# Optimization experiments

Measured on AMD Instinct MI355X. Metric: run time of the kernel, lower is better.

## Reference

```python
import jax, jax.numpy as jnp
import numpy as np

B, L, D_IN, D_MODEL, H = 8, 1024, 256, 512, 8
D_HEAD = D_MODEL // H


def setup_inputs() -> dict:
    key = jax.random.key(0)
    ks = jax.random.split(key, 12)
    queries = jax.random.normal(ks[0], (B, L, D_IN), dtype=jnp.float32)
    keys_ = jax.random.normal(ks[1], (B, L, D_IN), dtype=jnp.float32)
    values = jax.random.normal(ks[2], (B, L, D_IN), dtype=jnp.float32)
    attention_mask = jnp.ones((B, L), dtype=jnp.int32)
    # binary symmetric-ish adjacency (sparse molecular graph style)
    adjacency_matrix = (jax.random.uniform(ks[3], (B, L, L)) < 0.05).astype(jnp.float32)
    distance_matrix = jax.random.uniform(ks[4], (B, L, L), dtype=jnp.float32) * 10.0
    s = 1.0 / np.sqrt(D_IN)
    W_q = jax.random.normal(ks[5], (D_MODEL, D_IN), dtype=jnp.float32) * s
    W_k = jax.random.normal(ks[6], (D_MODEL, D_IN), dtype=jnp.float32) * s
    W_v = jax.random.normal(ks[7], (D_MODEL, D_IN), dtype=jnp.float32) * s
    W_o = jax.random.normal(ks[8], (D_MODEL, D_MODEL), dtype=jnp.float32) / np.sqrt(D_MODEL)
    lambda_a = jax.random.normal(ks[9], (H,), dtype=jnp.float32) * 0.1
    lambda_d = jax.random.normal(ks[10], (H,), dtype=jnp.float32) * 0.1
    return {"queries": queries, "keys": keys_, "values": values,
            "attention_mask": attention_mask, "adjacency_matrix": adjacency_matrix,
            "distance_matrix": distance_matrix, "W_q": W_q, "W_k": W_k,
            "W_v": W_v, "W_o": W_o, "lambda_a": lambda_a, "lambda_d": lambda_d}


def _split_heads(x):
    # (b, l, d_model) -> (b, h, l, d_head)
    b, l, _ = x.shape
    return x.reshape(b, l, H, D_HEAD).transpose(0, 2, 1, 3)


def reference(queries, keys, values, attention_mask, adjacency_matrix,
              distance_matrix, W_q, W_k, W_v, W_o, lambda_a, lambda_d):
    Q = _split_heads(queries @ W_q.T)   # (b,h,l,d)
    K = _split_heads(keys @ W_k.T)
    V = _split_heads(values @ W_v.T)
    scores = jnp.einsum("bhqd,bhkd->bhqk", Q, K) / jnp.sqrt(jnp.asarray(D_HEAD, Q.dtype))
    # MSRSA: per-head learned scalars inject graph structure into the scores
    scores = (scores
              + lambda_a[None, :, None, None] * adjacency_matrix[:, None, :, :]
              + lambda_d[None, :, None, None] * distance_matrix[:, None, :, :])
    mask = attention_mask[:, None, None, :] > 0  # (b,1,1,l) key mask
    scores = jnp.where(mask, scores, jnp.asarray(-1e9, scores.dtype))
    attn_weight = jax.nn.softmax(scores, axis=-1)  # (b,h,l,l)
    out = jnp.einsum("bhqk,bhkd->bhqd", attn_weight, V)
    out = out.transpose(0, 2, 1, 3).reshape(queries.shape[0], queries.shape[1], D_MODEL)
    return out @ W_o.T
```

## Files before the change

### kernel.cpp

```cpp
#include <hip/hip_runtime.h>
#include <hip/hip_fp16.h>

#define BB 8
#define LL 1024
#define DIN 256
#define DM 512
#define HH 8
#define DH 64

typedef __attribute__((ext_vector_type(8))) short bf16x8;
typedef __attribute__((ext_vector_type(4))) float f32x4;
typedef _Float16 h2f __attribute__((ext_vector_type(2)));

__device__ __forceinline__ unsigned short f2bf(float f) {
  union { float f; unsigned u; } c; c.f = f;
  unsigned u = c.u;
  return (unsigned short)((u + 0x7fffu + ((u >> 16) & 1u)) >> 16);
}

#if defined(__has_builtin)
#if __has_builtin(__builtin_amdgcn_cvt_pk_bf16_f32)
#define HAS_PK_BF16 1
#endif
#endif

#if defined(HAS_PK_BF16)
typedef __bf16 bf2 __attribute__((ext_vector_type(2)));
__device__ __forceinline__ unsigned pk2(float lo, float hi) {
  union { bf2 v; unsigned u; } c;
  c.v = __builtin_amdgcn_cvt_pk_bf16_f32(lo, hi);
  return c.u;
}
#else
__device__ __forceinline__ unsigned pk2(float lo, float hi) {
  return ((unsigned)f2bf(hi) << 16) | f2bf(lo);
}
#endif

__device__ __forceinline__ float biasdot(unsigned u, h2f lam, float t) {
#if defined(__HIP_DEVICE_COMPILE__)
  union { unsigned v; h2f hv; } c; c.v = u;
  return __builtin_amdgcn_fdot2(c.hv, lam, t, false);
#else
  (void)u; (void)lam;
  return t;
#endif
}

__device__ __forceinline__ unsigned pkh(float a, float d) {
  return (unsigned)__half_as_ushort(__float2half_rn(a)) |
         ((unsigned)__half_as_ushort(__float2half_rn(d)) << 16);
}

__device__ __forceinline__ void async_copy16(void* lds, const void* g) {
  __builtin_amdgcn_global_load_lds(
      (const __attribute__((address_space(1))) unsigned*)g,
      (__attribute__((address_space(3))) unsigned*)lds, 16, 0, 0);
}

__global__ __launch_bounds__(256) void prep(
    const float* __restrict__ qin, const float* __restrict__ kin,
    const float* __restrict__ vin,
    const float* __restrict__ wq, const float* __restrict__ wk,
    const float* __restrict__ wv, const float* __restrict__ wo,
    const int* __restrict__ msk,
    const float* __restrict__ adj, const float* __restrict__ dis,
    unsigned short* __restrict__ xq, unsigned short* __restrict__ xk,
    unsigned short* __restrict__ xv,
    unsigned short* __restrict__ wqb, unsigned short* __restrict__ wkb,
    unsigned short* __restrict__ wvb, unsigned short* __restrict__ wob,
    float* __restrict__ mad, unsigned* __restrict__ bp)
{
  int t = blockIdx.x * 256 + threadIdx.x;
  const int XS = 524288, WS = 32768;
  if (t < 3 * XS) {
    int seg = t >> 19, off = t & (XS - 1);
    const float* s = (seg == 0) ? qin : (seg == 1) ? kin : vin;
    unsigned short* d = (seg == 0) ? xq : (seg == 1) ? xk : xv;
    float4 f = ((const float4*)s)[off];
    uint2 o = { pk2(f.x, f.y), pk2(f.z, f.w) };
    ((uint2*)d)[off] = o;
    return;
  }
  t -= 3 * XS;
  if (t < 3 * WS) {
    int seg = t >> 15, off = t & (WS - 1);
    const float* s = (seg == 0) ? wq : (seg == 1) ? wk : wv;
    unsigned short* d = (seg == 0) ? wqb : (seg == 1) ? wkb : wvb;
    float4 f = ((const float4*)s)[off];
    uint2 o = { pk2(f.x, f.y), pk2(f.z, f.w) };
    ((uint2*)d)[off] = o;
    return;
  }
  t -= 3 * WS;
  if (t < 65536) {
    float4 f = ((const float4*)wo)[t];
    uint2 o = { pk2(f.x, f.y), pk2(f.z, f.w) };
    ((uint2*)wob)[t] = o;
    return;
  }
  t -= 65536;
  if (t < 2048) {
    int4 m = ((const int4*)msk)[t];
    float4 f = { m.x ? 0.0f : -30000.0f, m.y ? 0.0f : -30000.0f,
                 m.z ? 0.0f : -30000.0f, m.w ? 0.0f : -30000.0f };
    ((float4*)mad)[t] = f;
    return;
  }
  t -= 2048;
  float4 a4 = ((const float4*)adj)[t];
  float4 d4 = ((const float4*)dis)[t];
  uint4 o = { pkh(a4.x, d4.x), pkh(a4.y, d4.y), pkh(a4.z, d4.z), pkh(a4.w, d4.w) };
  ((uint4*)bp)[t] = o;
}

__global__ __launch_bounds__(256) void qkv_proj(
    const unsigned short* __restrict__ xq, const unsigned short* __restrict__ xk,
    const unsigned short* __restrict__ xv,
    const unsigned short* __restrict__ wqb, const unsigned short* __restrict__ wkb,
    const unsigned short* __restrict__ wvb,
    unsigned short* __restrict__ qb, unsigned short* __restrict__ kb,
    unsigned short* __restrict__ vt)
{
  const int t = blockIdx.z;
  const unsigned short* __restrict__ X = (t == 0) ? xq : (t == 1) ? xk : xv;
  const unsigned short* __restrict__ W = (t == 0) ? wqb : (t == 1) ? wkb : wvb;
  const int m0 = blockIdx.y * 128;
  const int h  = blockIdx.x;
  __shared__ __align__(16) char arena[24576];
  const int tid = threadIdx.x;
  const int wid = tid >> 6;
  const int lane = tid & 63;
  const int lo = lane & 15;
  const int quad = lane >> 4;

  f32x4 acc[2][4];
#pragma unroll
  for (int mi = 0; mi < 2; ++mi)
#pragma unroll
    for (int ni = 0; ni < 4; ++ni) acc[mi][ni] = (f32x4)0.0f;

#pragma unroll
  for (int j = 0; j < 2; ++j) {
    int id = j * 256 + tid, r = id >> 2, c = id & 3;
    async_copy16(arena + j * 4096 + wid * 1024,
                 X + (size_t)(m0 + r) * DIN + ((c ^ (r & 3)) * 8));
  }
  {
    int id = tid, r = id >> 2, c = id & 3;
    async_copy16(arena + 16384 + wid * 1024,
                 W + (size_t)(h * 64 + r) * DIN + ((c ^ (r & 3)) * 8));
  }
  __syncthreads();

  for (int it = 0; it < 8; ++it) {
    const int p = it & 1;
    if (it < 7) {
      const int kk = (it + 1) * 32, q = 1 - p;
#pragma unroll
      for (int j = 0; j < 2; ++j) {
        int id = j * 256 + tid, r = id >> 2, c = id & 3;
        async_copy16(arena + q * 8192 + j * 4096 + wid * 1024,
                     X + (size_t)(m0 + r) * DIN + kk + ((c ^ (r & 3)) * 8));
      }
      {
        int id = tid, r = id >> 2, c = id & 3;
        async_copy16(arena + 16384 + q * 4096 + wid * 1024,
                     W + (size_t)(h * 64 + r) * DIN + kk + ((c ^ (r & 3)) * 8));
      }
    }
    const unsigned short* Ab = (const unsigned short*)(arena + p * 8192);
    const unsigned short* Bb = (const unsigned short*)(arena + 16384 + p * 4096);
    bf16x8 a[2], bfr[4];
#pragma unroll
    for (int mi = 0; mi < 2; ++mi) {
      int R = wid * 32 + mi * 16 + lo;
      a[mi] = *(const bf16x8*)&Ab[R * 32 + ((quad ^ (R & 3)) * 8)];
    }
#pragma unroll
    for (int ni = 0; ni < 4; ++ni) {
      int N = ni * 16 + lo;
      bfr[ni] = *(const bf16x8*)&Bb[N * 32 + ((quad ^ (N & 3)) * 8)];
    }
#pragma unroll
    for (int mi = 0; mi < 2; ++mi)
#pragma unroll
      for (int ni = 0; ni < 4; ++ni)
        acc[mi][ni] = __builtin_amdgcn_mfma_f32_16x16x32_bf16(
            a[mi], bfr[ni], acc[mi][ni], 0, 0, 0);
    __syncthreads();
  }

  const int b = m0 >> 10;
  const int lbase0 = (m0 & 1023) + wid * 32;
  if (t < 2) {
    unsigned short* dstp = (t == 0) ? qb : kb;
#pragma unroll
    for (int mi = 0; mi < 2; ++mi)
#pragma unroll
      for (int ni = 0; ni < 4; ++ni) {
        int d = ni * 16 + lo;
#pragma unroll
        for (int r = 0; r < 4; ++r) {
          int lb = lbase0 + mi * 16 + quad * 4 + r;
          dstp[((size_t)(b * HH + h) * LL + lb) * DH + d] = f2bf(acc[mi][ni][r]);
        }
      }
  } else {
#pragma unroll
    for (int mi = 0; mi < 2; ++mi)
#pragma unroll
      for (int ni = 0; ni < 4; ++ni) {
        int d = ni * 16 + lo;
        int lb = lbase0 + quad * 8 + mi * 4;
        uint2 o = { pk2(acc[mi][ni][0], acc[mi][ni][1]),
                    pk2(acc[mi][ni][2], acc[mi][ni][3]) };
        *(uint2*)&vt[((size_t)(b * HH + h) * DH + d) * LL + lb] = o;
      }
  }
}

__global__ __launch_bounds__(256) void attn(
    const unsigned short* __restrict__ qb, const unsigned short* __restrict__ kb,
    const unsigned short* __restrict__ vt,
    const float* __restrict__ mad, const unsigned* __restrict__ bp,
    const float* __restrict__ la_, const float* __restrict__ ld_,
    unsigned short* __restrict__ ao)
{
  const int bi = blockIdx.x;
  const int b  = bi & 7;
  const int hg = (bi >> 3) & 3;
  const int q0 = (bi >> 5) * 32;
  const int tid = threadIdx.x;
  const int wid = tid >> 6;
  const int lane = tid & 63;
  const int lo = lane & 15;
  const int quad = lane >> 4;
  const int h  = hg * 2 + (wid & 1);
  const int kh = wid >> 1;
  const int bh = b * HH + h;

  __shared__ __align__(16) char arena[49152];
  float* mgbuf = (float*)arena;

  const float LOG2E = 1.44269504f;
  const float la2 = la_[h] * LOG2E, ld2 = ld_[h] * LOG2E;
  const float sc2 = 0.125f * LOG2E;
  h2f lam2;
  lam2.x = (_Float16)la2;
  lam2.y = (_Float16)ld2;

  const unsigned short* qp = qb + ((size_t)bh * LL + q0) * DH;
  bf16x8 qB[2][2];
#pragma unroll
  for (int nj = 0; nj < 2; ++nj)
#pragma unroll
    for (int ki = 0; ki < 2; ++ki)
      qB[nj][ki] = *(const bf16x8*)&qp[(nj * 16 + lo) * DH + ki * 32 + quad * 8];

  const unsigned short* kp = kb + (size_t)bh * LL * DH;
  const unsigned short* vp = vt + (size_t)bh * DH * LL;
  const unsigned* bpp = bp + ((size_t)b * LL + q0) * LL;
  const float* mp = mad + b * LL;

  f32x4 o[4][2];
  float rs[2] = {0.0f, 0.0f};
#pragma unroll
  for (int md = 0; md < 4; ++md)
#pragma unroll
    for (int nj = 0; nj < 2; ++nj) o[md][nj] = (f32x4)0.0f;

  const int kbeg = kh * (LL / 2);
  const int r8 = lane >> 3, p8 = lane & 7;

  {
    const unsigned short* kg = kp + (size_t)kbeg * DH;
#pragma unroll
    for (int j = 0; j < 4; ++j)
      async_copy16(arena + wid * 4096 + j * 1024,
                   kg + (j * 8 + r8) * 64 + ((p8 ^ r8) * 8));
    if ((wid & 1) == 0) {
      const int khs = wid >> 1;
      const unsigned* bg = bpp + khs * (LL / 2);
#pragma unroll
      for (int j = 0; j < 4; ++j)
        async_copy16(arena + 32768 + khs * 4096 + j * 1024,
                     bg + (size_t)(j * 8 + r8) * LL + ((p8 ^ r8) * 4));
    }
  }
  __syncthreads();

  for (int jt = 0; jt < 16; ++jt) {
    const int p = jt & 1;
    const int k0 = kbeg + jt * 32;

    if (jt < 15) {
      const int kn = k0 + 32, q = 1 - p;
      const unsigned short* kg = kp + (size_t)kn * DH;
#pragma unroll
      for (int j = 0; j < 4; ++j)
        async_copy16(arena + q * 16384 + wid * 4096 + j * 1024,
                     kg + (j * 8 + r8) * 64 + ((p8 ^ r8) * 8));
      if ((wid & 1) == 0) {
        const int khs = wid >> 1;
        const unsigned* bg = bpp + khs * (LL / 2) + (jt + 1) * 32;
#pragma unroll
        for (int j = 0; j < 4; ++j)
          async_copy16(arena + 32768 + q * 8192 + khs * 4096 + j * 1024,
                       bg + (size_t)(j * 8 + r8) * LL + ((p8 ^ r8) * 4));
      }
    }

    bf16x8 vA[4];
#pragma unroll
    for (int md = 0; md < 4; ++md)
      vA[md] = *(const bf16x8*)&vp[(md * 16 + lo) * LL + k0 + quad * 8];
    f32x4 msv[2];
#pragma unroll
    for (int mi = 0; mi < 2; ++mi)
      msv[mi] = *(const f32x4*)&mp[k0 + mi * 16 + quad * 4];

    asm volatile("" ::: "memory");

    const unsigned short* kbf = (const unsigned short*)(arena + p * 16384) + wid * 2048;
    bf16x8 kA[2][2];
#pragma unroll
    for (int mi = 0; mi < 2; ++mi)
#pragma unroll
      for (int ki = 0; ki < 2; ++ki)
        kA[mi][ki] = *(const bf16x8*)&kbf[(mi * 16 + lo) * 64 +
                                          (((ki * 4 + quad) ^ (lo & 7)) * 8)];
    f32x4 s[2][2];
#pragma unroll
    for (int mi = 0; mi < 2; ++mi)
#pragma unroll
      for (int nj = 0; nj < 2; ++nj) s[mi][nj] = (f32x4)0.0f;
#pragma unroll
    for (int ki = 0; ki < 2; ++ki)
#pragma unroll
      for (int mi = 0; mi < 2; ++mi)
#pragma unroll
        for (int nj = 0; nj < 2; ++nj)
          s[mi][nj] = __builtin_amdgcn_mfma_f32_16x16x32_bf16(
              kA[mi][ki], qB[nj][ki], s[mi][nj], 0, 0, 0);

    const unsigned* bbf = (const unsigned*)(arena + 32768 + p * 8192) + kh * 1024;
    unsigned pw[2][4];
#pragma unroll
    for (int mi = 0; mi < 2; ++mi)
#pragma unroll
      for (int nj = 0; nj < 2; ++nj) {
        uint4 u = *(const uint4*)&bbf[(nj * 16 + lo) * 32 +
                                      (((mi * 4 + quad) ^ (lo & 7)) * 4)];
        float p4[4];
#pragma unroll
        for (int r = 0; r < 4; ++r) {
          float tb = fmaf(s[mi][nj][r], sc2, msv[mi][r]);
          p4[r] = __builtin_amdgcn_exp2f(biasdot(u[r], lam2, tb));
        }
        rs[nj] += (p4[0] + p4[1]) + (p4[2] + p4[3]);
        pw[nj][mi * 2]     = pk2(p4[0], p4[1]);
        pw[nj][mi * 2 + 1] = pk2(p4[2], p4[3]);
      }
    bf16x8 pB[2];
#pragma unroll
    for (int nj = 0; nj < 2; ++nj) {
      union { unsigned u[4]; bf16x8 v; } pc;
      pc.u[0] = pw[nj][0]; pc.u[1] = pw[nj][1];
      pc.u[2] = pw[nj][2]; pc.u[3] = pw[nj][3];
      pB[nj] = pc.v;
    }

#pragma unroll
    for (int md = 0; md < 4; ++md)
#pragma unroll
      for (int nj = 0; nj < 2; ++nj)
        o[md][nj] = __builtin_amdgcn_mfma_f32_16x16x32_bf16(
            vA[md], pB[nj], o[md][nj], 0, 0, 0);

    __syncthreads();
  }

  const int hs = wid & 1;
  if (kh == 1) {
#pragma unroll
    for (int md = 0; md < 4; ++md)
#pragma unroll
      for (int nj = 0; nj < 2; ++nj)
#pragma unroll
        for (int r = 0; r < 4; ++r)
          mgbuf[hs * 2176 + ((md * 2 + nj) * 4 + r) * 64 + lane] = o[md][nj][r];
    mgbuf[hs * 2176 + 32 * 64 + lane] = rs[0];
    mgbuf[hs * 2176 + 33 * 64 + lane] = rs[1];
  }
  __syncthreads();
  if (kh == 0) {
#pragma unroll
    for (int md = 0; md < 4; ++md)
#pragma unroll
      for (int nj = 0; nj < 2; ++nj)
#pragma unroll
        for (int r = 0; r < 4; ++r)
          o[md][nj][r] += mgbuf[hs * 2176 + ((md * 2 + nj) * 4 + r) * 64 + lane];
    rs[0] += mgbuf[hs * 2176 + 32 * 64 + lane];
    rs[1] += mgbuf[hs * 2176 + 33 * 64 + lane];
    float inv[2];
#pragma unroll
    for (int nj = 0; nj < 2; ++nj) {
      rs[nj] += __shfl_xor(rs[nj], 16);
      rs[nj] += __shfl_xor(rs[nj], 32);
      inv[nj] = __builtin_amdgcn_rcpf(rs[nj]);
    }
#pragma unroll
    for (int md = 0; md < 4; ++md)
#pragma unroll
      for (int nj = 0; nj < 2; ++nj) {
        int l = q0 + nj * 16 + lo;
        uint2 st = { pk2(o[md][nj][0] * inv[nj], o[md][nj][1] * inv[nj]),
                     pk2(o[md][nj][2] * inv[nj], o[md][nj][3] * inv[nj]) };
        *(uint2*)&ao[((size_t)b * LL + l) * DM + h * DH + md * 16 + quad * 4] = st;
      }
  }
}

__global__ __launch_bounds__(256) void oproj(
    const unsigned short* __restrict__ ao, const unsigned short* __restrict__ wob,
    float* __restrict__ out)
{
  const int m0 = blockIdx.y * 128;
  const int n0 = blockIdx.x * 64;
  __shared__ __align__(16) char arena[24576];
  const int tid = threadIdx.x;
  const int wid = tid >> 6;
  const int lane = tid & 63;
  const int lo = lane & 15;
  const int quad = lane >> 4;

  f32x4 acc[2][4];
#pragma unroll
  for (int mi = 0; mi < 2; ++mi)
#pragma unroll
    for (int ni = 0; ni < 4; ++ni) acc[mi][ni] = (f32x4)0.0f;

#pragma unroll
  for (int j = 0; j < 2; ++j) {
    int id = j * 256 + tid, r = id >> 2, c = id & 3;
    async_copy16(arena + j * 4096 + wid * 1024,
                 ao + (size_t)(m0 + r) * DM + ((c ^ (r & 3)) * 8));
  }
  {
    int id = tid, r = id >> 2, c = id & 3;
    async_copy16(arena + 16384 + wid * 1024,
                 wob + (size_t)(n0 + r) * DM + ((c ^ (r & 3)) * 8));
  }
  __syncthreads();

  for (int it = 0; it < 16; ++it) {
    const int p = it & 1;
    if (it < 15) {
      const int kk = (it + 1) * 32, q = 1 - p;
#pragma unroll
      for (int j = 0; j < 2; ++j) {
        int id = j * 256 + tid, r = id >> 2, c = id & 3;
        async_copy16(arena + q * 8192 + j * 4096 + wid * 1024,
                     ao + (size_t)(m0 + r) * DM + kk + ((c ^ (r & 3)) * 8));
      }
      {
        int id = tid, r = id >> 2, c = id & 3;
        async_copy16(arena + 16384 + q * 4096 + wid * 1024,
                     wob + (size_t)(n0 + r) * DM + kk + ((c ^ (r & 3)) * 8));
      }
    }
    const unsigned short* Ab = (const unsigned short*)(arena + p * 8192);
    const unsigned short* Bb = (const unsigned short*)(arena + 16384 + p * 4096);
    bf16x8 a[2], bfr[4];
#pragma unroll
    for (int mi = 0; mi < 2; ++mi) {
      int R = wid * 32 + mi * 16 + lo;
      a[mi] = *(const bf16x8*)&Ab[R * 32 + ((quad ^ (R & 3)) * 8)];
    }
#pragma unroll
    for (int ni = 0; ni < 4; ++ni) {
      int N = ni * 16 + lo;
      bfr[ni] = *(const bf16x8*)&Bb[N * 32 + ((quad ^ (N & 3)) * 8)];
    }
#pragma unroll
    for (int mi = 0; mi < 2; ++mi)
#pragma unroll
      for (int ni = 0; ni < 4; ++ni)
        acc[mi][ni] = __builtin_amdgcn_mfma_f32_16x16x32_bf16(
            a[mi], bfr[ni], acc[mi][ni], 0, 0, 0);
    __syncthreads();
  }

#pragma unroll
  for (int mi = 0; mi < 2; ++mi)
#pragma unroll
    for (int ni = 0; ni < 4; ++ni)
#pragma unroll
      for (int r = 0; r < 4; ++r)
        out[(size_t)(m0 + wid * 32 + mi * 16 + quad * 4 + r) * DM +
            n0 + ni * 16 + lo] = acc[mi][ni][r];
}

extern "C" void kernel_launch(void* const* d_in, const int* in_sizes, int n_in,
                              void* d_out, int out_size, void* d_ws, size_t ws_size,
                              hipStream_t stream) {
  const float* qin = (const float*)d_in[0];
  const float* kin = (const float*)d_in[1];
  const float* vin = (const float*)d_in[2];
  const int*   msk = (const int*)d_in[3];
  const float* adj = (const float*)d_in[4];
  const float* dis = (const float*)d_in[5];
  const float* wq  = (const float*)d_in[6];
  const float* wk  = (const float*)d_in[7];
  const float* wv  = (const float*)d_in[8];
  const float* wo  = (const float*)d_in[9];
  const float* la  = (const float*)d_in[10];
  const float* ld  = (const float*)d_in[11];
  float* out = (float*)d_out;

  const size_t tensb = (size_t)BB * HH * LL * DH;
  const size_t xsz   = (size_t)BB * LL * DIN;
  unsigned short* qb  = (unsigned short*)d_ws;
  unsigned short* kb  = qb + tensb;
  unsigned short* vt  = kb + tensb;
  unsigned short* ao  = vt + tensb;
  unsigned short* xq  = ao;
  unsigned short* xk  = ao + xsz;
  unsigned short* xv  = ao + tensb;
  unsigned short* wqb = xv + xsz;
  unsigned short* wkb = wqb + (size_t)DM * DIN;
  unsigned short* wvb = wkb + (size_t)DM * DIN;
  unsigned short* wob = wvb + (size_t)DM * DIN;
  float*          mdd = (float*)(wob + (size_t)DM * DM);
  unsigned*       bpk = (unsigned*)(mdd + (size_t)BB * LL);

  prep<<<dim3(14984), 256, 0, stream>>>(qin, kin, vin, wq, wk, wv, wo, msk,
                                        adj, dis,
                                        xq, xk, xv, wqb, wkb, wvb, wob, mdd, bpk);
  qkv_proj<<<dim3(8, 64, 3), 256, 0, stream>>>(xq, xk, xv, wqb, wkb, wvb, qb, kb, vt);
  attn<<<dim3(1024), 256, 0, stream>>>(qb, kb, vt, mdd, bpk, la, ld, ao);
  oproj<<<dim3(8, 64), 256, 0, stream>>>(ao, wob, out);
}
```

Before: 230.9 us.

## Give each wave private LDS buffers and drop per-tile block barriers

Each wave now gets its own 16KB LDS region holding double-buffered K and bias-packet tiles, instead of sharing buffers across the block. This lets the per-iteration __syncthreads be replaced by per-wave s_waitcnt vmcnt waits on the async copies, and the prefetch is moved after the V and mask global loads. The cost is LDS growing from 48KB to 64KB per block, which may lower occupancy, and bias tiles are now loaded redundantly by both head-waves of a pair. The hand-coded vmcnt counts depend on the exact number of outstanding loads, so a compiler reordering could make them wrong.

```diff
diff --git a/kernel.cpp b/kernel.cpp
--- a/kernel.cpp
+++ b/kernel.cpp
@@ -240,7 +240,8 @@
   const int kh = wid >> 1;
   const int bh = b * HH + h;
 
-  __shared__ __align__(16) char arena[49152];
+  __shared__ __align__(16) char arena[65536];
+  char* kpriv = arena + wid * 16384;
   float* mgbuf = (float*)arena;
 
   const float LOG2E = 1.44269504f;
@@ -277,40 +278,18 @@
     const unsigned short* kg = kp + (size_t)kbeg * DH;
 #pragma unroll
     for (int j = 0; j < 4; ++j)
-      async_copy16(arena + wid * 4096 + j * 1024,
-                   kg + (j * 8 + r8) * 64 + ((p8 ^ r8) * 8));
-    if ((wid & 1) == 0) {
-      const int khs = wid >> 1;
-      const unsigned* bg = bpp + khs * (LL / 2);
-#pragma unroll
-      for (int j = 0; j < 4; ++j)
-        async_copy16(arena + 32768 + khs * 4096 + j * 1024,
-                     bg + (size_t)(j * 8 + r8) * LL + ((p8 ^ r8) * 4));
-    }
-  }
-  __syncthreads();
+      async_copy16(kpriv + j * 1024, kg + (j * 8 + r8) * 64 + ((p8 ^ r8) * 8));
+    const unsigned* bg = bpp + kh * (LL / 2);
+#pragma unroll
+    for (int j = 0; j < 4; ++j)
+      async_copy16(kpriv + 8192 + j * 1024,
+                   bg + (size_t)(j * 8 + r8) * LL + ((p8 ^ r8) * 4));
+  }
 
   for (int jt = 0; jt < 16; ++jt) {
     const int p = jt & 1;
     const int k0 = kbeg + jt * 32;
 
-    if (jt < 15) {
-      const int kn = k0 + 32, q = 1 - p;
-      const unsigned short* kg = kp + (size_t)kn * DH;
-#pragma unroll
-      for (int j = 0; j < 4; ++j)
-        async_copy16(arena + q * 16384 + wid * 4096 + j * 1024,
-                     kg + (j * 8 + r8) * 64 + ((p8 ^ r8) * 8));
-      if ((wid & 1) == 0) {
-        const int khs = wid >> 1;
-        const unsigned* bg = bpp + khs * (LL / 2) + (jt + 1) * 32;
-#pragma unroll
-        for (int j = 0; j < 4; ++j)
-          async_copy16(arena + 32768 + q * 8192 + khs * 4096 + j * 1024,
-                       bg + (size_t)(j * 8 + r8) * LL + ((p8 ^ r8) * 4));
-      }
-    }
-
     bf16x8 vA[4];
 #pragma unroll
     for (int md = 0; md < 4; ++md)
@@ -319,10 +298,27 @@
 #pragma unroll
     for (int mi = 0; mi < 2; ++mi)
       msv[mi] = *(const f32x4*)&mp[k0 + mi * 16 + quad * 4];
-
     asm volatile("" ::: "memory");
 
-    const unsigned short* kbf = (const unsigned short*)(arena + p * 16384) + wid * 2048;
+    if (jt < 15) {
+      const int pn = 1 - p;
+      const unsigned short* kg = kp + (size_t)(k0 + 32) * DH;
+#pragma unroll
+      for (int j = 0; j < 4; ++j)
+        async_copy16(kpriv + pn * 4096 + j * 1024,
+                     kg + (j * 8 + r8) * 64 + ((p8 ^ r8) * 8));
+      const unsigned* bg = bpp + kh * (LL / 2) + (jt + 1) * 32;
+#pragma unroll
+      for (int j = 0; j < 4; ++j)
+        async_copy16(kpriv + 8192 + pn * 4096 + j * 1024,
+                     bg + (size_t)(j * 8 + r8) * LL + ((p8 ^ r8) * 4));
+      asm volatile("" ::: "memory");
+      asm volatile("s_waitcnt vmcnt(14)" ::: "memory");
+    } else {
+      asm volatile("s_waitcnt vmcnt(6)" ::: "memory");
+    }
+
+    const unsigned short* kbf = (const unsigned short*)(kpriv + p * 4096);
     bf16x8 kA[2][2];
 #pragma unroll
     for (int mi = 0; mi < 2; ++mi)
@@ -344,7 +340,7 @@
           s[mi][nj] = __builtin_amdgcn_mfma_f32_16x16x32_bf16(
               kA[mi][ki], qB[nj][ki], s[mi][nj], 0, 0, 0);
 
-    const unsigned* bbf = (const unsigned*)(arena + 32768 + p * 8192) + kh * 1024;
+    const unsigned* bbf = (const unsigned*)(kpriv + 8192 + p * 4096);
     unsigned pw[2][4];
 #pragma unroll
     for (int mi = 0; mi < 2; ++mi)
@@ -377,10 +373,9 @@
       for (int nj = 0; nj < 2; ++nj)
         o[md][nj] = __builtin_amdgcn_mfma_f32_16x16x32_bf16(
             vA[md], pB[nj], o[md][nj], 0, 0, 0);
-
-    __syncthreads();
-  }
-
+  }
+
+  __syncthreads();
   const int hs = wid & 1;
   if (kh == 1) {
 #pragma unroll
```

Result: no change. 231.5 us (+0.3%).

## Preload full weight tile to LDS and use per-wave X buffers without barriers

Applied to the files above, without the earlier changes.

In both the QKV projection and output projection GEMMs, the whole weight tile for the block is loaded into LDS once up front. Each wave now streams its own private double-buffered slice of the activation rows, synchronising with s_waitcnt vmcnt instead of a block-wide __syncthreads every k-step. This removes the per-iteration barriers and repeated weight loads. In exchange, LDS use rises to 48KB and 80KB per block, which may lower occupancy, and correctness now rests on hand-written waitcnt ordering.

```diff
diff --git a/kernel.cpp b/kernel.cpp
--- a/kernel.cpp
+++ b/kernel.cpp
@@ -127,12 +127,13 @@
   const unsigned short* __restrict__ W = (t == 0) ? wqb : (t == 1) ? wkb : wvb;
   const int m0 = blockIdx.y * 128;
   const int h  = blockIdx.x;
-  __shared__ __align__(16) char arena[24576];
+  __shared__ __align__(16) char arena[49152];
   const int tid = threadIdx.x;
   const int wid = tid >> 6;
   const int lane = tid & 63;
   const int lo = lane & 15;
   const int quad = lane >> 4;
+  char* xpriv = arena + 32768 + wid * 4096;
 
   f32x4 acc[2][4];
 #pragma unroll
@@ -141,46 +142,47 @@
     for (int ni = 0; ni < 4; ++ni) acc[mi][ni] = (f32x4)0.0f;
 
 #pragma unroll
+  for (int j = 0; j < 8; ++j) {
+    int idx = j * 256 + tid, r = idx >> 5, c = idx & 31;
+    async_copy16(arena + j * 4096 + wid * 1024,
+                 W + (size_t)(h * 64 + r) * DIN + ((c ^ (r & 15)) * 8));
+  }
+#pragma unroll
   for (int j = 0; j < 2; ++j) {
-    int id = j * 256 + tid, r = id >> 2, c = id & 3;
-    async_copy16(arena + j * 4096 + wid * 1024,
-                 X + (size_t)(m0 + r) * DIN + ((c ^ (r & 3)) * 8));
-  }
-  {
-    int id = tid, r = id >> 2, c = id & 3;
-    async_copy16(arena + 16384 + wid * 1024,
-                 W + (size_t)(h * 64 + r) * DIN + ((c ^ (r & 3)) * 8));
+    int idx = j * 64 + lane, r = idx >> 2, c = idx & 3;
+    async_copy16(xpriv + j * 1024,
+                 X + (size_t)(m0 + wid * 32 + r) * DIN + ((c ^ (r & 3)) * 8));
   }
   __syncthreads();
 
+  const unsigned short* Wb = (const unsigned short*)arena;
   for (int it = 0; it < 8; ++it) {
     const int p = it & 1;
     if (it < 7) {
-      const int kk = (it + 1) * 32, q = 1 - p;
+      const int kk = (it + 1) * 32;
 #pragma unroll
       for (int j = 0; j < 2; ++j) {
-        int id = j * 256 + tid, r = id >> 2, c = id & 3;
-        async_copy16(arena + q * 8192 + j * 4096 + wid * 1024,
-                     X + (size_t)(m0 + r) * DIN + kk + ((c ^ (r & 3)) * 8));
-      }
-      {
-        int id = tid, r = id >> 2, c = id & 3;
-        async_copy16(arena + 16384 + q * 4096 + wid * 1024,
-                     W + (size_t)(h * 64 + r) * DIN + kk + ((c ^ (r & 3)) * 8));
-      }
-    }
-    const unsigned short* Ab = (const unsigned short*)(arena + p * 8192);
-    const unsigned short* Bb = (const unsigned short*)(arena + 16384 + p * 4096);
+        int idx = j * 64 + lane, r = idx >> 2, c = idx & 3;
+        async_copy16(xpriv + (1 - p) * 2048 + j * 1024,
+                     X + (size_t)(m0 + wid * 32 + r) * DIN + kk +
+                         ((c ^ (r & 3)) * 8));
+      }
+      asm volatile("" ::: "memory");
+      asm volatile("s_waitcnt vmcnt(2)" ::: "memory");
+    } else {
+      asm volatile("s_waitcnt vmcnt(0)" ::: "memory");
+    }
+    const unsigned short* Ab = (const unsigned short*)(xpriv + p * 2048);
     bf16x8 a[2], bfr[4];
 #pragma unroll
     for (int mi = 0; mi < 2; ++mi) {
-      int R = wid * 32 + mi * 16 + lo;
+      int R = mi * 16 + lo;
       a[mi] = *(const bf16x8*)&Ab[R * 32 + ((quad ^ (R & 3)) * 8)];
     }
 #pragma unroll
     for (int ni = 0; ni < 4; ++ni) {
       int N = ni * 16 + lo;
-      bfr[ni] = *(const bf16x8*)&Bb[N * 32 + ((quad ^ (N & 3)) * 8)];
+      bfr[ni] = *(const bf16x8*)&Wb[N * 256 + (((it * 4 + quad) ^ (N & 15)) * 8)];
     }
 #pragma unroll
     for (int mi = 0; mi < 2; ++mi)
@@ -188,7 +190,6 @@
       for (int ni = 0; ni < 4; ++ni)
         acc[mi][ni] = __builtin_amdgcn_mfma_f32_16x16x32_bf16(
             a[mi], bfr[ni], acc[mi][ni], 0, 0, 0);
-    __syncthreads();
   }
 
   const int b = m0 >> 10;
@@ -429,12 +430,13 @@
 {
   const int m0 = blockIdx.y * 128;
   const int n0 = blockIdx.x * 64;
-  __shared__ __align__(16) char arena[24576];
+  __shared__ __align__(16) char arena[81920];
   const int tid = threadIdx.x;
   const int wid = tid >> 6;
   const int lane = tid & 63;
   const int lo = lane & 15;
   const int quad = lane >> 4;
+  char* xpriv = arena + 65536 + wid * 4096;
 
   f32x4 acc[2][4];
 #pragma unroll
@@ -443,46 +445,47 @@
     for (int ni = 0; ni < 4; ++ni) acc[mi][ni] = (f32x4)0.0f;
 
 #pragma unroll
+  for (int j = 0; j < 16; ++j) {
+    int idx = j * 256 + tid, r = idx >> 6, c = idx & 63;
+    async_copy16(arena + j * 4096 + wid * 1024,
+                 wob + (size_t)(n0 + r) * DM + ((c ^ (r & 15)) * 8));
+  }
+#pragma unroll
   for (int j = 0; j < 2; ++j) {
-    int id = j * 256 + tid, r = id >> 2, c = id & 3;
-    async_copy16(arena + j * 4096 + wid * 1024,
-                 ao + (size_t)(m0 + r) * DM + ((c ^ (r & 3)) * 8));
-  }
-  {
-    int id = tid, r = id >> 2, c = id & 3;
-    async_copy16(arena + 16384 + wid * 1024,
-                 wob + (size_t)(n0 + r) * DM + ((c ^ (r & 3)) * 8));
+    int idx = j * 64 + lane, r = idx >> 2, c = idx & 3;
+    async_copy16(xpriv + j * 1024,
+                 ao + (size_t)(m0 + wid * 32 + r) * DM + ((c ^ (r & 3)) * 8));
   }
   __syncthreads();
 
+  const unsigned short* Wb = (const unsigned short*)arena;
   for (int it = 0; it < 16; ++it) {
     const int p = it & 1;
     if (it < 15) {
-      const int kk = (it + 1) * 32, q = 1 - p;
+      const int kk = (it + 1) * 32;
 #pragma unroll
       for (int j = 0; j < 2; ++j) {
-        int id = j * 256 + tid, r = id >> 2, c = id & 3;
-        async_copy16(arena + q * 8192 + j * 4096 + wid * 1024,
-                     ao + (size_t)(m0 + r) * DM + kk + ((c ^ (r & 3)) * 8));
-      }
-      {
-        int id = tid, r = id >> 2, c = id & 3;
-        async_copy16(arena + 16384 + q * 4096 + wid * 1024,
-                     wob + (size_t)(n0 + r) * DM + kk + ((c ^ (r & 3)) * 8));
-      }
-    }
-    const unsigned short* Ab = (const unsigned short*)(arena + p * 8192);
-    const unsigned short* Bb = (const unsigned short*)(arena + 16384 + p * 4096);
+        int idx = j * 64 + lane, r = idx >> 2, c = idx & 3;
+        async_copy16(xpriv + (1 - p) * 2048 + j * 1024,
+                     ao + (size_t)(m0 + wid * 32 + r) * DM + kk +
+                         ((c ^ (r & 3)) * 8));
+      }
+      asm volatile("" ::: "memory");
+      asm volatile("s_waitcnt vmcnt(2)" ::: "memory");
+    } else {
+      asm volatile("s_waitcnt vmcnt(0)" ::: "memory");
+    }
+    const unsigned short* Ab = (const unsigned short*)(xpriv + p * 2048);
     bf16x8 a[2], bfr[4];
 #pragma unroll
     for (int mi = 0; mi < 2; ++mi) {
-      int R = wid * 32 + mi * 16 + lo;
+      int R = mi * 16 + lo;
       a[mi] = *(const bf16x8*)&Ab[R * 32 + ((quad ^ (R & 3)) * 8)];
     }
 #pragma unroll
     for (int ni = 0; ni < 4; ++ni) {
       int N = ni * 16 + lo;
-      bfr[ni] = *(const bf16x8*)&Bb[N * 32 + ((quad ^ (N & 3)) * 8)];
+      bfr[ni] = *(const bf16x8*)&Wb[N * 512 + (((it * 4 + quad) ^ (N & 15)) * 8)];
     }
 #pragma unroll
     for (int mi = 0; mi < 2; ++mi)
@@ -490,7 +493,6 @@
       for (int ni = 0; ni < 4; ++ni)
         acc[mi][ni] = __builtin_amdgcn_mfma_f32_16x16x32_bf16(
             a[mi], bfr[ni], acc[mi][ni], 0, 0, 0);
-    __syncthreads();
   }
 
 #pragma unroll
```

Result: no change. 229.1 us (-0.8%).
